# Optimization experiments

Measured on AMD Instinct MI355X. Metric: run time of the kernel, lower is better.

## Reference

```python
import jax, jax.numpy as jnp
import numpy as np

MAX_DISP = 24  # matches init_kwargs


def setup_inputs() -> dict:
    key = jax.random.key(0)
    k1, k2 = jax.random.split(key)
    B, H, W, C = 2, 256, 256, 16
    left = jax.random.normal(k1, (B, H, W, C), dtype=jnp.float32)
    right = jax.random.normal(k2, (B, H, W, C), dtype=jnp.float32)
    return {"left": left, "right": right}


def reference(left, right):
    # left/right: [B, H, W, C]. Builds concat cost volume [B, 2*max_disp, H, W, 2C].
    # For disparity i in [-max_disp, max_disp): out[d, :, w] pairs left[w] with
    # right[w - i]; positions where w - i falls outside [0, W) are zero-padded
    # (both the left and right halves, matching tf.pad of the concatenated slice).
    W = left.shape[2]
    disps = jnp.arange(-MAX_DISP, MAX_DISP)              # [2D]
    idx = jnp.arange(W)[None, :] - disps[:, None]        # [2D, W] source col in right
    valid = (idx >= 0) & (idx < W)                       # [2D, W]
    idx_c = jnp.clip(idx, 0, W - 1)
    mask = valid[None, None, :, :, None].astype(left.dtype)  # [1,1,2D,W,1]
    r = right[:, :, idx_c, :] * mask                     # [B,H,2D,W,C]
    l = left[:, :, None, :, :] * mask                    # [B,H,2D,W,C]
    vol = jnp.concatenate([l, r], axis=-1)               # [B,H,2D,W,2C]
    return jnp.transpose(vol, (0, 2, 1, 3, 4))           # [B,2D,H,W,2C]
```

## Files before the change

kernel.cpp:

```cpp
#include <hip/hip_runtime.h>


#define MAXD 24
#define ND   48
#define HH   256
#define WW   256

__global__ __launch_bounds__(1024) void FeatureVolume_68762426409246_kernel(
    const float4* __restrict__ left,
    const float4* __restrict__ right,
    float4* __restrict__ out) {
    __shared__ float4 lds[2 * WW * 4];

    const unsigned int bh  = blockIdx.x;
    const unsigned int b   = bh >> 8;
    const unsigned int tid = threadIdx.x;

    const unsigned int row_base = bh * (WW * 4);
    lds[tid]          = left [row_base + tid];
    lds[WW * 4 + tid] = right[row_base + tid];
    __syncthreads();

    const unsigned int out_base = (b * (ND * HH) + (bh & 255u)) * (WW * 8);

    const unsigned int total = ND * WW * 8;
    for (unsigned int idx = tid; idx < total; idx += 1024) {
        unsigned int c4 = idx & 7u;
        unsigned int w  = (idx >> 3) & 255u;
        unsigned int d  = idx >> 11;

        int src_w  = (int)w - ((int)d - MAXD);
        bool valid = ((unsigned)src_w < (unsigned)WW);

        int col_r = min(max(src_w, 0), WW - 1);
        unsigned int col  = (c4 < 4u) ? w : (unsigned)col_r;
        unsigned int half = (c4 < 4u) ? 0u : (unsigned)(WW * 4);

        float4 v = lds[half + col * 4u + (c4 & 3u)];
        float  m = valid ? 1.0f : 0.0f;

        out[out_base + d * (HH * WW * 8) + (idx & 2047u)] =
            make_float4(v.x * m, v.y * m, v.z * m, v.w * m);
    }
}

extern "C" void kernel_launch(void* const* d_in, const int* in_sizes, int n_in,
                              void* d_out, int out_size, void* d_ws, size_t ws_size,
                              hipStream_t stream) {
    const float4* left  = (const float4*)d_in[0];
    const float4* right = (const float4*)d_in[1];
    float4* out = (float4*)d_out;

    FeatureVolume_68762426409246_kernel<<<2 * HH, 1024, 0, stream>>>(
        left, right, out);
}
```

Baseline: 152.4 us.

## Use zero-padded right row in LDS and keep left values in registers

The right row is staged in LDS with zero padding on both sides, so out-of-range disparities read zeros with no clamping or masking. Each thread keeps its two left float4 values in registers and loops over disparities with fixed output columns, software-prefetching the next right value and selecting zeros for left where the pair is invalid. Per-element index arithmetic and multiplies are removed, and the launch bounds request higher occupancy. The kernel is store-bound, so the benefit may be limited to lower instruction overhead.

```diff
diff --git a/kernel.cpp b/kernel.cpp
--- a/kernel.cpp
+++ b/kernel.cpp
@@ -5,42 +5,60 @@
 #define ND   48
 #define HH   256
 #define WW   256
+#define SLICE_F4 (HH * WW * 8)
 
-__global__ __launch_bounds__(1024) void FeatureVolume_68762426409246_kernel(
+__global__ __launch_bounds__(1024, 8) void FeatureVolume_68762426409246_kernel(
     const float4* __restrict__ left,
     const float4* __restrict__ right,
     float4* __restrict__ out) {
-    __shared__ float4 lds[2 * WW * 4];
+    __shared__ float4 rpad[1216];
 
-    const unsigned int bh  = blockIdx.x;
-    const unsigned int b   = bh >> 8;
-    const unsigned int tid = threadIdx.x;
+    const unsigned bh  = blockIdx.x;
+    const unsigned b   = bh >> 8;
+    const unsigned t   = threadIdx.x;
+    const unsigned c4  = t & 7u;
+    const unsigned cc  = t & 3u;
+    const unsigned wlo = t >> 3;
+    const unsigned row = bh << 10;
+    const float4 Z = make_float4(0.f, 0.f, 0.f, 0.f);
 
-    const unsigned int row_base = bh * (WW * 4);
-    lds[tid]          = left [row_base + tid];
-    lds[WW * 4 + tid] = right[row_base + tid];
+    if (t < 96u)            rpad[t] = Z;
+    else if (t < 192u)      rpad[1024u + t] = Z;
+    rpad[96u + t] = right[row + t];
+
+    const float4 L0 = left[row + (wlo << 2) + cc];
+    const float4 L1 = left[row + ((wlo + 128u) << 2) + cc];
     __syncthreads();
 
-    const unsigned int out_base = (b * (ND * HH) + (bh & 255u)) * (WW * 8);
+    const bool isL   = (c4 < 4u);
+    const int  dmax0 = (int)wlo + MAXD;
+    const int  dmin1 = (int)wlo - 103;
 
-    const unsigned int total = ND * WW * 8;
-    for (unsigned int idx = tid; idx < total; idx += 1024) {
-        unsigned int c4 = idx & 7u;
-        unsigned int w  = (idx >> 3) & 255u;
-        unsigned int d  = idx >> 11;
+    unsigned a0 = (48u + wlo) * 4u + cc;
+    unsigned a1 = a0 + 512u;
 
-        int src_w  = (int)w - ((int)d - MAXD);
-        bool valid = ((unsigned)src_w < (unsigned)WW);
+    float4* op = out + (((size_t)(b * (ND * HH) + (bh & 255u))) << 11) + t;
 
-        int col_r = min(max(src_w, 0), WW - 1);
-        unsigned int col  = (c4 < 4u) ? w : (unsigned)col_r;
-        unsigned int half = (c4 < 4u) ? 0u : (unsigned)(WW * 4);
-
-        float4 v = lds[half + col * 4u + (c4 & 3u)];
-        float  m = valid ? 1.0f : 0.0f;
-
-        out[out_base + d * (HH * WW * 8) + (idx & 2047u)] =
-            make_float4(v.x * m, v.y * m, v.z * m, v.w * m);
+    float4 r0 = rpad[a0];
+    float4 r1 = rpad[a1];
+    #pragma unroll 4
+    for (int d = 0; d < ND - 1; ++d) {
+        a0 -= 4u; a1 -= 4u;
+        float4 n0 = rpad[a0];
+        float4 n1 = rpad[a1];
+        float4 x0 = isL ? ((d <= dmax0) ? L0 : Z) : r0;
+        float4 x1 = isL ? ((d >= dmin1) ? L1 : Z) : r1;
+        op[0]    = x0;
+        op[1024] = x1;
+        op += SLICE_F4;
+        r0 = n0; r1 = n1;
+    }
+    {
+        const int d = ND - 1;
+        float4 x0 = isL ? ((d <= dmax0) ? L0 : Z) : r0;
+        float4 x1 = isL ? ((d >= dmin1) ? L1 : Z) : r1;
+        op[0]    = x0;
+        op[1024] = x1;
     }
 }
 
```

Measured after the change: 150.4 us (median of 2 runs). No clear change (-1.3%).
